# Performance work log

Hardware: AMD Instinct MI355X
Metric: run time of the kernel (lower is better)

The kernel has to match this reference:

```python
import jax, jax.numpy as jnp
import numpy as np

B, S, D = 2, 2048, 1024
H, DH = 16, 64
LN_EPS = 1e-5
NEG_INF = -1e9


def setup_inputs() -> dict:
    key = jax.random.key(0)
    ks = jax.random.split(key, 8)
    x = jax.random.normal(ks[0], (B, S, D), dtype=jnp.float32)
    mask = jax.random.randint(ks[1], (B, 1, S, S), 0, 5) == 0
    sc = 1.0 / np.sqrt(D)
    W_attn = jax.random.normal(ks[2], (D, 3 * H * DH), dtype=jnp.float32) * sc
    b_attn = jnp.zeros((3 * H * DH,), dtype=jnp.float32)
    W_out = jax.random.normal(ks[3], (H * DH, D), dtype=jnp.float32) * sc
    b_out = jnp.zeros((D,), dtype=jnp.float32)
    ln_g = jnp.ones((D,), dtype=jnp.float32)
    ln_b = jnp.zeros((D,), dtype=jnp.float32)
    return {"x": x, "W_attn": W_attn, "b_attn": b_attn, "W_out": W_out,
            "b_out": b_out, "ln_g": ln_g, "ln_b": ln_b, "mask": mask}


def reference(x, W_attn, b_attn, W_out, b_out, ln_g, ln_b, mask):
    bs, s, _ = x.shape
    qkv = x @ W_attn + b_attn                      # [b, s, 3*H*DH]
    q, k, v = jnp.split(qkv, 3, axis=-1)
    q = q.reshape(bs, s, H, DH)
    k = k.reshape(bs, s, H, DH)
    v = v.reshape(bs, s, H, DH)
    scores = jnp.einsum('bqhd,bkhd->bhqk', q, k) / np.sqrt(DH)
    scores = jnp.where(mask, NEG_INF, scores)
    probs = jax.nn.softmax(scores, axis=-1)        # attn_p = 0 -> dropout is identity
    attn = jnp.einsum('bhqk,bkhd->bqhd', probs, v).reshape(bs, s, H * DH)
    y = x + (attn @ W_out + b_out)                 # resid_p = 0
    mu = jnp.mean(y, axis=-1, keepdims=True)
    var = jnp.mean((y - mu) ** 2, axis=-1, keepdims=True)
    return (y - mu) * jax.lax.rsqrt(var + LN_EPS) * ln_g + ln_b
```

## Files before the change

kernel.cpp:

```cpp
#include <hip/hip_runtime.h>
#include <math.h>

#define BB 2
#define SS 2048
#define DD 1024
#define HH 16
#define DHD 64
#define N3 3072
#define LN_EPS 1e-5f

#define PLANE (BB*HH*SS*DHD)

typedef __attribute__((ext_vector_type(8))) short bf16x8;
typedef __attribute__((ext_vector_type(4))) float f32x4;
typedef unsigned int u32;
typedef unsigned short ushort_t;

static __device__ __forceinline__ short f2bf(float f) {
  union { float f; unsigned u; } a;
  a.f = f;
  unsigned r = a.u + 0x7fffu + ((a.u >> 16) & 1u);
  return (short)(r >> 16);
}

static __device__ __forceinline__ void gload_lds16(const void* g, void* l) {
  __builtin_amdgcn_global_load_lds(
      (const __attribute__((address_space(1))) u32*)g,
      (__attribute__((address_space(3))) u32*)l, 16, 0, 0);
}

__global__ __launch_bounds__(256) void conv_bf16_kernel(
    const float* __restrict__ in, ushort_t* __restrict__ out) {
  int i = (blockIdx.x * 256 + threadIdx.x) * 8;
  float4 a = *(const float4*)&in[i];
  float4 b = *(const float4*)&in[i + 4];
  short s[8] = {f2bf(a.x), f2bf(a.y), f2bf(a.z), f2bf(a.w),
                f2bf(b.x), f2bf(b.y), f2bf(b.z), f2bf(b.w)};
  *(bf16x8*)&out[i] = *(bf16x8*)s;
}

__global__ __launch_bounds__(256) void transpose_bf16_kernel(
    const float* __restrict__ W, ushort_t* __restrict__ Wt, int K, int N) {
  __shared__ float tile[64][65];
  const int tid = threadIdx.x;
  const int nb = blockIdx.x * 64, kb = blockIdx.y * 64;
  #pragma unroll
  for (int i = 0; i < 4; ++i) {
    int idx = tid + i * 256;
    int r = idx >> 4, c = (idx & 15) * 4;
    float4 v = *(const float4*)&W[(size_t)(kb + r) * N + nb + c];
    tile[r][c] = v.x; tile[r][c + 1] = v.y; tile[r][c + 2] = v.z; tile[r][c + 3] = v.w;
  }
  __syncthreads();
  #pragma unroll
  for (int i = 0; i < 4; ++i) {
    int idx = tid + i * 256;
    int n = idx >> 4, k = (idx & 15) * 4;
    short4 s;
    s.x = f2bf(tile[k][n]); s.y = f2bf(tile[k + 1][n]);
    s.z = f2bf(tile[k + 2][n]); s.w = f2bf(tile[k + 3][n]);
    *(short4*)&Wt[(size_t)(nb + n) * K + kb + k] = s;
  }
}

__global__ __launch_bounds__(256) void pack_mask_kernel(
    const int* __restrict__ mask, unsigned long long* __restrict__ bits) {
  size_t g = (size_t)blockIdx.x * 256 + threadIdx.x;
  int m = mask[g];
  unsigned long long b = __ballot(m != 0);
  if ((threadIdx.x & 63) == 0) bits[g >> 6] = b;
}

#define GEMM_MAIN(Aptr, Btptr, Kdim)                                          \
  __shared__ ushort_t As[128 * 64];                                           \
  __shared__ ushort_t Bs[128 * 64];                                           \
  const int tid = threadIdx.x;                                                \
  const int wave = tid >> 6, lane = tid & 63;                                 \
  const int lane16 = lane & 15, quad = lane >> 4;                             \
  const int wm = wave & 1, wn = wave >> 1;                                    \
  const int bm = blockIdx.y * 128, bn = blockIdx.x * 128;                     \
  const int srow = lane >> 3;                                                 \
  const int sg = (lane & 7) ^ srow;                                           \
  f32x4 acc[4][4];                                                            \
  _Pragma("unroll") for (int i = 0; i < 4; ++i)                               \
    _Pragma("unroll") for (int j = 0; j < 4; ++j)                             \
      acc[i][j] = (f32x4){0.f, 0.f, 0.f, 0.f};                                \
  const ushort_t* agp[4];                                                     \
  const ushort_t* bgp[4];                                                     \
  _Pragma("unroll") for (int i = 0; i < 4; ++i) {                             \
    int seg = wave * 4 + i;                                                   \
    int r = seg * 8 + srow;                                                   \
    agp[i] = Aptr + (size_t)(bm + r) * Kdim + sg * 8;                         \
    bgp[i] = Btptr + (size_t)(bn + r) * Kdim + sg * 8;                        \
  }                                                                           \
  for (int k0 = 0; k0 < Kdim; k0 += 64) {                                     \
    _Pragma("unroll") for (int i = 0; i < 4; ++i) {                           \
      int seg = wave * 4 + i;                                                 \
      gload_lds16(agp[i] + k0, &As[seg * 512]);                               \
      gload_lds16(bgp[i] + k0, &Bs[seg * 512]);                               \
    }                                                                         \
    __syncthreads();                                                          \
    _Pragma("unroll") for (int ks = 0; ks < 2; ++ks) {                        \
      bf16x8 af[4], bfr[4];                                                   \
      _Pragma("unroll") for (int mt = 0; mt < 4; ++mt) {                      \
        int ra = wm * 64 + mt * 16 + lane16;                                  \
        int kc = ks * 4 + quad;                                               \
        af[mt] = *(const bf16x8*)&As[ra * 64 + ((kc ^ (ra & 7)) * 8)];        \
      }                                                                       \
      _Pragma("unroll") for (int nt = 0; nt < 4; ++nt) {                      \
        int rb = wn * 64 + nt * 16 + lane16;                                  \
        int kc = ks * 4 + quad;                                               \
        bfr[nt] = *(const bf16x8*)&Bs[rb * 64 + ((kc ^ (rb & 7)) * 8)];       \
      }                                                                       \
      _Pragma("unroll") for (int mt = 0; mt < 4; ++mt)                        \
        _Pragma("unroll") for (int nt = 0; nt < 4; ++nt)                      \
          acc[mt][nt] = __builtin_amdgcn_mfma_f32_16x16x32_bf16(              \
              af[mt], bfr[nt], acc[mt][nt], 0, 0, 0);                         \
    }                                                                         \
    __syncthreads();                                                          \
  }

__global__ __launch_bounds__(256) void gemm_qkv_mfma(
    const ushort_t* __restrict__ A, const ushort_t* __restrict__ Bt,
    const float* __restrict__ bias, ushort_t* __restrict__ qkvh) {
  GEMM_MAIN(A, Bt, DD)
  #pragma unroll
  for (int nt = 0; nt < 4; ++nt) {
    int col = bn + wn * 64 + nt * 16 + lane16;
    int which = col >> 10, hcol = col & 1023;
    int head = hcol >> 6, d = hcol & 63;
    float bv = bias[col];
    ushort_t* plane = qkvh + (size_t)which * PLANE;
    #pragma unroll
    for (int mt = 0; mt < 4; ++mt) {
      #pragma unroll
      for (int reg = 0; reg < 4; ++reg) {
        int row = bm + wm * 64 + mt * 16 + quad * 4 + reg;
        int bb = row >> 11, ss = row & (SS - 1);
        plane[((size_t)(bb * HH + head) * SS + ss) * DHD + d] =
            (ushort_t)f2bf(acc[mt][nt][reg] + bv);
      }
    }
  }
}

__global__ __launch_bounds__(256) void gemm_proj_mfma(
    const ushort_t* __restrict__ A, const ushort_t* __restrict__ Bt,
    const float* __restrict__ bias, const float* __restrict__ xres,
    float* __restrict__ Y) {
  GEMM_MAIN(A, Bt, DD)
  #pragma unroll
  for (int nt = 0; nt < 4; ++nt) {
    int col = bn + wn * 64 + nt * 16 + lane16;
    float bv = bias[col];
    #pragma unroll
    for (int mt = 0; mt < 4; ++mt) {
      #pragma unroll
      for (int reg = 0; reg < 4; ++reg) {
        int row = bm + wm * 64 + mt * 16 + quad * 4 + reg;
        Y[(size_t)row * DD + col] =
            acc[mt][nt][reg] + bv + xres[(size_t)row * DD + col];
      }
    }
  }
}

__global__ __launch_bounds__(256) void attn_mfma_kernel(
    const ushort_t* __restrict__ qh, const ushort_t* __restrict__ kh,
    const ushort_t* __restrict__ vh, const u32* __restrict__ mbits,
    ushort_t* __restrict__ attn_out) {
  __shared__ __align__(16) short Kt[64][76];
  __shared__ __align__(16) short Vt[64][76];
  __shared__ __align__(16) short Pt[4][16][76];

  const int tid = threadIdx.x;
  const int wave = tid >> 6, lane = tid & 63;
  const int lane16 = lane & 15, quad = lane >> 4;

  const int qt = blockIdx.x & 31;
  const int bh = blockIdx.x >> 5;
  const int bbi = bh >> 4, hhi = bh & 15;
  const size_t head_base = (size_t)bh * SS * DHD;
  const int q0 = qt * 64 + wave * 16;
  const int qrow_g = q0 + quad * 4;

  bf16x8 qf[2];
  {
    const ushort_t* qsrc = &qh[head_base + (size_t)(q0 + lane16) * DHD + quad * 8];
    #pragma unroll
    for (int ks = 0; ks < 2; ++ks) {
      bf16x8 r = *(const bf16x8*)&qsrc[ks * 32];
      #pragma unroll
      for (int e = 0; e < 8; ++e) {
        union { u32 u; float f; } c;
        c.u = ((u32)(ushort_t)r[e]) << 16;
        c.f *= 0.125f;
        r[e] = f2bf(c.f);
      }
      qf[ks] = r;
    }
  }

  bf16x8 onesf;
  #pragma unroll
  for (int e = 0; e < 8; ++e) onesf[e] = (short)0x3F80;

  f32x4 acc[4];
  f32x4 lacc = (f32x4){0.f, 0.f, 0.f, 0.f};
  #pragma unroll
  for (int dt = 0; dt < 4; ++dt) acc[dt] = (f32x4){0.f, 0.f, 0.f, 0.f};

  const u32* mrow_base = mbits + ((size_t)(bbi * SS) + qrow_g) * 64;

  for (int kt = 0; kt < SS; kt += 64) {
    __syncthreads();
    #pragma unroll
    for (int i = 0; i < 2; ++i) {
      int g = tid + i * 256;
      int r = g >> 3, c = (g & 7) * 8;
      *(bf16x8*)&Kt[r][c] = *(const bf16x8*)&kh[head_base + (size_t)(kt + r) * DHD + c];
    }
    {
      int c = tid & 63;
      int rb = (tid >> 6) * 16;
      #pragma unroll
      for (int i = 0; i < 4; ++i) {
        int r0 = rb + i * 4;
        const ushort_t* vsrc = &vh[head_base + (size_t)(kt + r0) * DHD + c];
        short4 s4;
        s4.x = (short)vsrc[0];
        s4.y = (short)vsrc[DHD];
        s4.z = (short)vsrc[2 * DHD];
        s4.w = (short)vsrc[3 * DHD];
        *(short4*)&Vt[c][r0] = s4;
      }
    }
    uint2 mw[4];
    #pragma unroll
    for (int reg = 0; reg < 4; ++reg)
      mw[reg] = *(const uint2*)&mrow_base[(size_t)reg * 64 + (kt >> 5)];
    __syncthreads();

    f32x4 sc[4];
    #pragma unroll
    for (int nt = 0; nt < 4; ++nt) {
      sc[nt] = (f32x4){0.f, 0.f, 0.f, 0.f};
      #pragma unroll
      for (int ks = 0; ks < 2; ++ks) {
        bf16x8 kf = *(const bf16x8*)&Kt[nt * 16 + lane16][ks * 32 + quad * 8];
        sc[nt] = __builtin_amdgcn_mfma_f32_16x16x32_bf16(qf[ks], kf, sc[nt], 0, 0, 0);
      }
    }

    #pragma unroll
    for (int reg = 0; reg < 4; ++reg) {
      u32 tl = mw[reg].x >> lane16;
      u32 th = mw[reg].y >> lane16;
      float e0 = (tl & 1u)       ? 0.f : __expf(sc[0][reg]);
      float e1 = (tl & 0x10000u) ? 0.f : __expf(sc[1][reg]);
      float e2 = (th & 1u)       ? 0.f : __expf(sc[2][reg]);
      float e3 = (th & 0x10000u) ? 0.f : __expf(sc[3][reg]);
      Pt[wave][quad * 4 + reg][ 0 + lane16] = f2bf(e0);
      Pt[wave][quad * 4 + reg][16 + lane16] = f2bf(e1);
      Pt[wave][quad * 4 + reg][32 + lane16] = f2bf(e2);
      Pt[wave][quad * 4 + reg][48 + lane16] = f2bf(e3);
    }
    __syncthreads();

    #pragma unroll
    for (int ks = 0; ks < 2; ++ks) {
      bf16x8 pf = *(const bf16x8*)&Pt[wave][lane16][ks * 32 + quad * 8];
      lacc = __builtin_amdgcn_mfma_f32_16x16x32_bf16(pf, onesf, lacc, 0, 0, 0);
      #pragma unroll
      for (int dt = 0; dt < 4; ++dt) {
        bf16x8 vf = *(const bf16x8*)&Vt[dt * 16 + lane16][ks * 32 + quad * 8];
        acc[dt] = __builtin_amdgcn_mfma_f32_16x16x32_bf16(pf, vf, acc[dt], 0, 0, 0);
      }
    }
  }

  #pragma unroll
  for (int reg = 0; reg < 4; ++reg) {
    float inv = 1.0f / lacc[reg];
    ushort_t* orow = &attn_out[((size_t)(bbi * SS) + qrow_g + reg) * DD
                               + hhi * DHD + lane16];
    #pragma unroll
    for (int dt = 0; dt < 4; ++dt)
      orow[dt * 16] = (ushort_t)f2bf(acc[dt][reg] * inv);
  }
}

__global__ __launch_bounds__(256) void ln_kernel(
    float* __restrict__ Y, const float* __restrict__ g,
    const float* __restrict__ bta) {
  const int r = blockIdx.x;
  const int tid = threadIdx.x;
  float4 v = *(const float4*)&Y[(size_t)r * DD + tid * 4];
  float sum = v.x + v.y + v.z + v.w;
  float sq = v.x * v.x + v.y * v.y + v.z * v.z + v.w * v.w;
  #pragma unroll
  for (int off = 32; off; off >>= 1) {
    sum += __shfl_down(sum, off);
    sq += __shfl_down(sq, off);
  }
  __shared__ float ps[4], pq[4];
  __shared__ float mu_s, rs_s;
  const int wave = tid >> 6;
  if ((tid & 63) == 0) { ps[wave] = sum; pq[wave] = sq; }
  __syncthreads();
  if (tid == 0) {
    float s = ps[0] + ps[1] + ps[2] + ps[3];
    float qq = pq[0] + pq[1] + pq[2] + pq[3];
    float mu = s * (1.0f / DD);
    float var = qq * (1.0f / DD) - mu * mu;
    mu_s = mu;
    rs_s = rsqrtf(var + LN_EPS);
  }
  __syncthreads();
  const float mu = mu_s, rs = rs_s;
  float4 g4 = *(const float4*)&g[tid * 4];
  float4 b4 = *(const float4*)&bta[tid * 4];
  float4 ov;
  ov.x = (v.x - mu) * rs * g4.x + b4.x;
  ov.y = (v.y - mu) * rs * g4.y + b4.y;
  ov.z = (v.z - mu) * rs * g4.z + b4.z;
  ov.w = (v.w - mu) * rs * g4.w + b4.w;
  *(float4*)&Y[(size_t)r * DD + tid * 4] = ov;
}

extern "C" void kernel_launch(void* const* d_in, const int* in_sizes, int n_in,
                              void* d_out, int out_size, void* d_ws, size_t ws_size,
                              hipStream_t stream) {
  const float* x      = (const float*)d_in[0];
  const float* W_attn = (const float*)d_in[1];
  const float* b_attn = (const float*)d_in[2];
  const float* W_out  = (const float*)d_in[3];
  const float* b_out  = (const float*)d_in[4];
  const float* ln_g   = (const float*)d_in[5];
  const float* ln_b   = (const float*)d_in[6];
  const int*   mask   = (const int*)d_in[7];
  float* out = (float*)d_out;
  ushort_t* ws = (ushort_t*)d_ws;

  ushort_t* xb    = ws;
  ushort_t* watt  = xb + (size_t)BB * SS * DD;
  ushort_t* wot   = watt + (size_t)N3 * DD;
  ushort_t* qh    = wot + (size_t)DD * DD;
  ushort_t* kh    = qh + (size_t)PLANE;
  ushort_t* vh    = kh + (size_t)PLANE;
  ushort_t* attnb = vh + (size_t)PLANE;
  u32* mbits      = (u32*)(attnb + (size_t)BB * SS * DD);

  conv_bf16_kernel<<<dim3((BB * SS * DD) / (256 * 8)), 256, 0, stream>>>(x, xb);
  transpose_bf16_kernel<<<dim3(N3 / 64, DD / 64), 256, 0, stream>>>(W_attn, watt, DD, N3);
  transpose_bf16_kernel<<<dim3(DD / 64, DD / 64), 256, 0, stream>>>(W_out, wot, DD, DD);
  pack_mask_kernel<<<dim3((BB * SS * SS) / 256), 256, 0, stream>>>(
      mask, (unsigned long long*)mbits);

  gemm_qkv_mfma<<<dim3(N3 / 128, (BB * SS) / 128), 256, 0, stream>>>(
      xb, watt, b_attn, qh);
  attn_mfma_kernel<<<dim3(BB * HH * (SS / 64)), 256, 0, stream>>>(
      qh, kh, vh, mbits, attnb);
  gemm_proj_mfma<<<dim3(DD / 128, (BB * SS) / 128), 256, 0, stream>>>(
      attnb, wot, b_out, x, out);
  ln_kernel<<<dim3(BB * SS), 256, 0, stream>>>(out, ln_g, ln_b);
}
```

Baseline: 277.9 us.

## Prefetch next K/V/mask tile into registers and drop per-wave P barrier

Loads the next iteration's K, V and mask words into registers while the current tile is computed, then stores them to LDS at the top of the loop. This hides global memory latency behind the MFMA and exp work. It also removes the block barrier after writing the per-wave probability tile, since each wave reads only its own slice, and switches to a cheaper round-half-up bf16 conversion. These changes add register pressure, relax the ordering of the probability tile, and shift rounding slightly.

```diff
diff --git a/kernel.cpp b/kernel.cpp
--- a/kernel.cpp
+++ b/kernel.cpp
@@ -21,6 +21,12 @@
   a.f = f;
   unsigned r = a.u + 0x7fffu + ((a.u >> 16) & 1u);
   return (short)(r >> 16);
+}
+
+static __device__ __forceinline__ short f2bf_rhu(float f) {
+  union { float f; unsigned u; } a;
+  a.f = f;
+  return (short)((a.u + 0x8000u) >> 16);
 }
 
 static __device__ __forceinline__ void gload_lds16(const void* g, void* l) {
@@ -212,34 +218,63 @@
 
   const u32* mrow_base = mbits + ((size_t)(bbi * SS) + qrow_g) * 64;
 
+  const int kg_r = tid >> 3;
+  const int kg_c = (tid & 7) * 8;
+  const int vs_c = tid & 63;
+  const int vs_rb = (tid >> 6) * 16;
+
+  bf16x8 kreg[2];
+  short4 vreg[4];
+  uint2 mwn[4];
+  {
+    #pragma unroll
+    for (int i = 0; i < 2; ++i)
+      kreg[i] = *(const bf16x8*)&kh[head_base + (size_t)(kg_r + i * 32) * DHD + kg_c];
+    #pragma unroll
+    for (int i = 0; i < 4; ++i) {
+      int r0 = vs_rb + i * 4;
+      const ushort_t* vsrc = &vh[head_base + (size_t)r0 * DHD + vs_c];
+      vreg[i].x = (short)vsrc[0];
+      vreg[i].y = (short)vsrc[DHD];
+      vreg[i].z = (short)vsrc[2 * DHD];
+      vreg[i].w = (short)vsrc[3 * DHD];
+    }
+    #pragma unroll
+    for (int reg = 0; reg < 4; ++reg)
+      mwn[reg] = *(const uint2*)&mrow_base[(size_t)reg * 64];
+  }
+
   for (int kt = 0; kt < SS; kt += 64) {
     __syncthreads();
     #pragma unroll
-    for (int i = 0; i < 2; ++i) {
-      int g = tid + i * 256;
-      int r = g >> 3, c = (g & 7) * 8;
-      *(bf16x8*)&Kt[r][c] = *(const bf16x8*)&kh[head_base + (size_t)(kt + r) * DHD + c];
-    }
-    {
-      int c = tid & 63;
-      int rb = (tid >> 6) * 16;
+    for (int i = 0; i < 2; ++i)
+      *(bf16x8*)&Kt[kg_r + i * 32][kg_c] = kreg[i];
+    #pragma unroll
+    for (int i = 0; i < 4; ++i)
+      *(short4*)&Vt[vs_c][vs_rb + i * 4] = vreg[i];
+    uint2 mwc[4];
+    #pragma unroll
+    for (int reg = 0; reg < 4; ++reg) mwc[reg] = mwn[reg];
+    __syncthreads();
+
+    const int kt2 = kt + 64;
+    if (kt2 < SS) {
+      #pragma unroll
+      for (int i = 0; i < 2; ++i)
+        kreg[i] = *(const bf16x8*)&kh[head_base + (size_t)(kt2 + kg_r + i * 32) * DHD + kg_c];
       #pragma unroll
       for (int i = 0; i < 4; ++i) {
-        int r0 = rb + i * 4;
-        const ushort_t* vsrc = &vh[head_base + (size_t)(kt + r0) * DHD + c];
-        short4 s4;
-        s4.x = (short)vsrc[0];
-        s4.y = (short)vsrc[DHD];
-        s4.z = (short)vsrc[2 * DHD];
-        s4.w = (short)vsrc[3 * DHD];
-        *(short4*)&Vt[c][r0] = s4;
-      }
-    }
-    uint2 mw[4];
-    #pragma unroll
-    for (int reg = 0; reg < 4; ++reg)
-      mw[reg] = *(const uint2*)&mrow_base[(size_t)reg * 64 + (kt >> 5)];
-    __syncthreads();
+        int r0 = kt2 + vs_rb + i * 4;
+        const ushort_t* vsrc = &vh[head_base + (size_t)r0 * DHD + vs_c];
+        vreg[i].x = (short)vsrc[0];
+        vreg[i].y = (short)vsrc[DHD];
+        vreg[i].z = (short)vsrc[2 * DHD];
+        vreg[i].w = (short)vsrc[3 * DHD];
+      }
+      #pragma unroll
+      for (int reg = 0; reg < 4; ++reg)
+        mwn[reg] = *(const uint2*)&mrow_base[(size_t)reg * 64 + (kt2 >> 5)];
+    }
 
     f32x4 sc[4];
     #pragma unroll
@@ -254,18 +289,17 @@
 
     #pragma unroll
     for (int reg = 0; reg < 4; ++reg) {
-      u32 tl = mw[reg].x >> lane16;
-      u32 th = mw[reg].y >> lane16;
+      u32 tl = mwc[reg].x >> lane16;
+      u32 th = mwc[reg].y >> lane16;
       float e0 = (tl & 1u)       ? 0.f : __expf(sc[0][reg]);
       float e1 = (tl & 0x10000u) ? 0.f : __expf(sc[1][reg]);
       float e2 = (th & 1u)       ? 0.f : __expf(sc[2][reg]);
       float e3 = (th & 0x10000u) ? 0.f : __expf(sc[3][reg]);
-      Pt[wave][quad * 4 + reg][ 0 + lane16] = f2bf(e0);
-      Pt[wave][quad * 4 + reg][16 + lane16] = f2bf(e1);
-      Pt[wave][quad * 4 + reg][32 + lane16] = f2bf(e2);
-      Pt[wave][quad * 4 + reg][48 + lane16] = f2bf(e3);
-    }
-    __syncthreads();
+      Pt[wave][quad * 4 + reg][ 0 + lane16] = f2bf_rhu(e0);
+      Pt[wave][quad * 4 + reg][16 + lane16] = f2bf_rhu(e1);
+      Pt[wave][quad * 4 + reg][32 + lane16] = f2bf_rhu(e2);
+      Pt[wave][quad * 4 + reg][48 + lane16] = f2bf_rhu(e3);
+    }
 
     #pragma unroll
     for (int ks = 0; ks < 2; ++ks) {
```

Result: no change. 272.7 us (-1.9%).
